# Kernel tuning notes

Measured on AMD Instinct MI355X. Metric: run time of the kernel, lower is better.

## Reference

```python
import jax, jax.numpy as jnp
import numpy as np

N_HEAD = 16


def setup_inputs() -> dict:
    key = jax.random.key(0)
    k1, k2, k3 = jax.random.split(key, 3)
    B, T, C = 4, 2048, 1024
    x = jax.random.normal(k1, (B, T, C), dtype=jnp.float32)
    W = jax.random.normal(k2, (3 * C, C), dtype=jnp.float32) * (1.0 / np.sqrt(C))
    b = jax.random.normal(k3, (3 * C,), dtype=jnp.float32) * 0.02
    return {"x": x, "W": W, "b": b, "input_pos": 0}


def reference(x, W, b, input_pos):
    # cache=False path; input_pos is unused (kept for signature fidelity).
    B, T, C = x.shape
    H = N_HEAD
    hs = C // H
    # Fused QKV projection: torch Linear is x @ W.T + b -> [B, T, 3C]
    qkv = (jnp.einsum('btc,oc->bto', x, W) + b).reshape(B, T, 3, H, hs)
    # q, k, v: [B, H, T, hs]
    q = jnp.transpose(qkv[:, :, 0], (0, 2, 1, 3))
    k = jnp.transpose(qkv[:, :, 1], (0, 2, 1, 3))
    v = jnp.transpose(qkv[:, :, 2], (0, 2, 1, 3))
    scale = hs ** (-0.5)
    # scores: [B, H, T, T]
    scores = jnp.einsum('bhqd,bhkd->bhqk', q, k) * scale
    causal = jnp.tril(jnp.ones((T, T), dtype=bool))
    scores = jnp.where(causal, scores, -jnp.inf)
    wei = jax.nn.softmax(scores, axis=-1)
    out = jnp.einsum('bhqk,bhkd->bhqd', wei, v)  # [B, H, T, hs]
    return jnp.transpose(out, (0, 2, 1, 3)).reshape(B, T, C)
```

## Files before the change

### kernel.cpp

```cpp
#include <hip/hip_runtime.h>
#include <stdint.h>

using s16x8 = __attribute__((ext_vector_type(8))) short;
using u16x8 = __attribute__((ext_vector_type(8))) unsigned short;
using f32x4 = __attribute__((ext_vector_type(4))) float;
using u32x2 = __attribute__((ext_vector_type(2))) uint32_t;

__device__ __forceinline__ unsigned short f2bf(float f) {
    union { float f; uint32_t u; } v; v.f = f;
    uint32_t u = (v.u + 0x7FFFu + ((v.u >> 16) & 1u)) >> 16;
    return (unsigned short)u;
}

#if defined(__has_builtin)
#if __has_builtin(__builtin_amdgcn_cvt_pk_bf16_f32)
#define HAS_PK_BF16 1
#endif
#if __has_builtin(__builtin_amdgcn_exp2f)
#define HAS_EXP2 1
#endif
#endif

__device__ __forceinline__ float ex2(float x) {
#ifdef HAS_EXP2
    return __builtin_amdgcn_exp2f(x);
#else
    float r; asm("v_exp_f32 %0, %1" : "=v"(r) : "v"(x)); return r;
#endif
}

__device__ __forceinline__ uint32_t pk2bf(float x, float y) {
#ifdef HAS_PK_BF16
    typedef __bf16 bf16x2 __attribute__((ext_vector_type(2)));
    union { bf16x2 v; uint32_t u; } c;
    c.v = __builtin_amdgcn_cvt_pk_bf16_f32(x, y);
    return c.u;
#else
    union { __bf16 v[2]; uint32_t u; } c;
    c.v[0] = (__bf16)x; c.v[1] = (__bf16)y;
    return c.u;
#endif
}

__device__ __forceinline__ f32x4 zero4() { f32x4 z = {0.f, 0.f, 0.f, 0.f}; return z; }

__device__ __forceinline__ void async16(const void* g, void* l) {
    __builtin_amdgcn_global_load_lds(
        reinterpret_cast<const uint32_t __attribute__((address_space(1)))*>(
            reinterpret_cast<uintptr_t>(g)),
        reinterpret_cast<uint32_t __attribute__((address_space(3)))*>(
            (uint32_t)reinterpret_cast<uintptr_t>(l)),
        16, 0, 0);
}

__global__ void cvt_bf16_2(const float* __restrict__ xa, unsigned short* __restrict__ oa, int na,
                           const float* __restrict__ xb, unsigned short* __restrict__ ob, int nb) {
    int i = (blockIdx.x * 256 + threadIdx.x) * 8;
    const float* in; unsigned short* out;
    if (i < na) { in = xa + i; out = oa + i; }
    else { int k = i - na; if (k >= nb) return; in = xb + k; out = ob + k; }
    f32x4 a = *(const f32x4*)(in);
    f32x4 c = *(const f32x4*)(in + 4);
    u16x8 o;
    o[0] = f2bf(a[0]); o[1] = f2bf(a[1]); o[2] = f2bf(a[2]); o[3] = f2bf(a[3]);
    o[4] = f2bf(c[0]); o[5] = f2bf(c[1]); o[6] = f2bf(c[2]); o[7] = f2bf(c[3]);
    *(u16x8*)(out) = o;
}

#define SC 0.18033688011112042f

__global__ __launch_bounds__(256, 2)
void qkv_gemm(const unsigned short* __restrict__ A,
              const unsigned short* __restrict__ Bw,
              const float* __restrict__ bias,
              unsigned short* __restrict__ Qo,
              unsigned short* __restrict__ Ko,
              unsigned short* __restrict__ Vto) {
    constexpr int Kd = 1024, T = 2048, H = 16;
    __shared__ __align__(16) unsigned short smem[128 * 136];
    unsigned short* const As = smem;
    unsigned short* const Bs = smem + 128 * 64;
    const int tid = threadIdx.x;
    const int wave = tid >> 6, lane = tid & 63;
    const int q4 = lane >> 4, l15 = lane & 15;
    const int bm = blockIdx.y * 128, bn = blockIdx.x * 128;
    const int wm = (wave >> 1) * 64, wn = (wave & 1) * 64;

    f32x4 acc[4][4];
#pragma unroll
    for (int a = 0; a < 4; ++a)
#pragma unroll
        for (int c = 0; c < 4; ++c) acc[a][c] = zero4();

    for (int k0 = 0; k0 < Kd; k0 += 64) {
#pragma unroll
        for (int r = 0; r < 4; ++r) {
            int u = r * 256 + tid;
            int row = u >> 3, su = (u & 7) ^ (row & 7);
            async16(A + (size_t)(bm + row) * Kd + k0 + su * 8, (char*)As + u * 16);
        }
#pragma unroll
        for (int r = 0; r < 4; ++r) {
            int u = r * 256 + tid;
            int row = u >> 3, su = (u & 7) ^ (row & 7);
            async16(Bw + (size_t)(bn + row) * Kd + k0 + su * 8, (char*)Bs + u * 16);
        }
        __syncthreads();
#pragma unroll
        for (int kt = 0; kt < 2; ++kt) {
            s16x8 af[4];
#pragma unroll
            for (int mt = 0; mt < 4; ++mt) {
                int row = wm + mt * 16 + l15;
                int uu = (kt * 4 + q4) ^ (row & 7);
                af[mt] = *(const s16x8*)(As + row * 64 + uu * 8);
            }
#pragma unroll
            for (int nt = 0; nt < 4; ++nt) {
                int row = wn + nt * 16 + l15;
                int uu = (kt * 4 + q4) ^ (row & 7);
                s16x8 bfv = *(const s16x8*)(Bs + row * 64 + uu * 8);
#pragma unroll
                for (int mt = 0; mt < 4; ++mt)
                    acc[mt][nt] = __builtin_amdgcn_mfma_f32_16x16x32_bf16(af[mt], bfv, acc[mt][nt], 0, 0, 0);
            }
        }
        __syncthreads();
    }
    if (bn >= 2048) {
#pragma unroll
        for (int nt = 0; nt < 4; ++nt) {
            int n = bn + wn + nt * 16 + l15;
            float bv = bias[n];
            int dl = wn + nt * 16 + l15;
#pragma unroll
            for (int mt = 0; mt < 4; ++mt)
#pragma unroll
                for (int i = 0; i < 4; ++i) {
                    int ml = wm + mt * 16 + 4 * q4 + i;
                    smem[dl * 136 + ml] = f2bf(acc[mt][nt][i] + bv);
                }
        }
        __syncthreads();
        const int bb = bm >> 11, t0 = bm & (T - 1);
#pragma unroll
        for (int rr = 0; rr < 8; ++rr) {
            int r = wave * 32 + rr * 4 + q4;
            int d = (bn - 2048) + r;
            int h = d >> 6, dd = d & 63;
            u16x8 v = *(const u16x8*)(smem + r * 136 + l15 * 8);
            *(u16x8*)(Vto + (((size_t)(bb * H + h)) * 64 + dd) * T + t0 + l15 * 8) = v;
        }
    } else {
#pragma unroll
        for (int nt = 0; nt < 4; ++nt) {
            int n = bn + wn + nt * 16 + l15;
            float bv = bias[n];
            int which = n >> 10, h = (n >> 6) & (H - 1), d = n & 63;
            unsigned short* dst = (which == 0) ? Qo : Ko;
            float scl = (which == 0) ? SC : 1.0f;
#pragma unroll
            for (int mt = 0; mt < 4; ++mt)
#pragma unroll
                for (int i = 0; i < 4; ++i) {
                    int m = bm + wm + mt * 16 + 4 * q4 + i;
                    int bb = m >> 11, t = m & (T - 1);
                    dst[((((size_t)bb * H + h) * T) + t) * 64 + d] = f2bf((acc[mt][nt][i] + bv) * scl);
                }
        }
    }
}

__global__ __launch_bounds__(256, 3)
void flash_attn(const unsigned short* __restrict__ Qg,
                const unsigned short* __restrict__ Kg,
                const unsigned short* __restrict__ Vtg,
                float* __restrict__ Out) {
    constexpr int T = 2048;
    __shared__ __align__(16) unsigned short Qs[128 * 64];
    __shared__ __align__(16) unsigned short Ks[2][64 * 64];
    __shared__ __align__(16) unsigned short Vt[2][64 * 64];

    const int tid = threadIdx.x;
    const int wave = tid >> 6, lane = tid & 63;
    const int q4 = lane >> 4, l15 = lane & 15;
    const int bh = blockIdx.x;
    const int qt = (int)gridDim.y - 1 - (int)blockIdx.y;
    const int b = bh >> 4, h = bh & 15;
    const int q0 = qt * 128;
    const unsigned short* qb = Qg + (size_t)bh * T * 64;
    const unsigned short* kb = Kg + (size_t)bh * T * 64;
    const unsigned short* vtb = Vtg + (size_t)bh * 64 * T;

#pragma unroll
    for (int r = 0; r < 4; ++r) {
        int u = r * 256 + tid;
        int row = u >> 3, su = (u & 7) ^ (row & 7);
        async16(qb + (size_t)(q0 + row) * 64 + su * 8, (char*)Qs + u * 16);
    }
#pragma unroll
    for (int r = 0; r < 2; ++r) {
        int u = r * 256 + tid;
        int row = u >> 3, su = (u & 7) ^ (row & 7);
        async16(kb + (size_t)row * 64 + su * 8, (char*)Ks[0] + u * 16);
        async16(vtb + (size_t)row * T + su * 8, (char*)Vt[0] + u * 16);
    }
    __syncthreads();
    s16x8 aq[2][2];
#pragma unroll
    for (int s = 0; s < 2; ++s)
#pragma unroll
        for (int kt = 0; kt < 2; ++kt) {
            int arow = s * 64 + wave * 16 + l15;
            int au = (kt * 4 + q4) ^ (arow & 7);
            aq[s][kt] = *(const s16x8*)(Qs + arow * 64 + au * 8);
        }
    __syncthreads();
    unsigned short* const Ps0 = Qs + (wave * 2 + 0) * 1024;
    unsigned short* const Ps1 = Qs + (wave * 2 + 1) * 1024;

    f32x4 oacc[2][4];
    float lsum[2] = {0.f, 0.f};
#pragma unroll
    for (int s = 0; s < 2; ++s)
#pragma unroll
        for (int ct = 0; ct < 4; ++ct) oacc[s][ct] = zero4();

    const int nkt = 2 * qt + 2;

    auto tile_step = [&](int j,
                         const unsigned short* __restrict__ kcur,
                         const unsigned short* __restrict__ vcur,
                         unsigned short* __restrict__ kd,
                         unsigned short* __restrict__ vd) {
        if (j + 1 < nkt) {
            const int cn = (j + 1) * 64;
#pragma unroll
            for (int r = 0; r < 2; ++r) {
                int u = r * 256 + tid;
                int row = u >> 3, su = (u & 7) ^ (row & 7);
                async16(kb + (size_t)(cn + row) * 64 + su * 8, (char*)kd + u * 16);
                async16(vtb + (size_t)row * T + cn + su * 8, (char*)vd + u * 16);
            }
        }
        const int c0 = j * 64;
        const bool alive0 = (j <= 2 * qt);

        f32x4 sv[2][4];
#pragma unroll
        for (int s = 0; s < 2; ++s)
#pragma unroll
            for (int t = 0; t < 4; ++t) sv[s][t] = zero4();
#pragma unroll
        for (int kt = 0; kt < 2; ++kt) {
#pragma unroll
            for (int t = 0; t < 4; ++t) {
                int krow = t * 16 + l15;
                int ku = (kt * 4 + q4) ^ (krow & 7);
                s16x8 ak = *(const s16x8*)(kcur + krow * 64 + ku * 8);
                sv[0][t] = __builtin_amdgcn_mfma_f32_16x16x32_bf16(ak, aq[0][kt], sv[0][t], 0, 0, 0);
                sv[1][t] = __builtin_amdgcn_mfma_f32_16x16x32_bf16(ak, aq[1][kt], sv[1][t], 0, 0, 0);
            }
        }

#pragma unroll
        for (int s = 0; s < 2; ++s) {
            if (s == 0 && !alive0) continue;
            const bool dg = (j == 2 * qt + s);
            unsigned short* const ps = (s == 0) ? Ps0 : Ps1;
            const int qrow = q0 + s * 64 + wave * 16 + l15;
#pragma unroll
            for (int t = 0; t < 4; ++t) {
                float p0 = ex2(sv[s][t][0]);
                float p1 = ex2(sv[s][t][1]);
                float p2 = ex2(sv[s][t][2]);
                float p3 = ex2(sv[s][t][3]);
                if (dg) {
                    int col = c0 + t * 16 + 4 * q4;
                    if (col + 0 > qrow) p0 = 0.f;
                    if (col + 1 > qrow) p1 = 0.f;
                    if (col + 2 > qrow) p2 = 0.f;
                    if (col + 3 > qrow) p3 = 0.f;
                }
                lsum[s] += (p0 + p1) + (p2 + p3);
                u32x2 w;
                w[0] = pk2bf(p0, p1);
                w[1] = pk2bf(p2, p3);
                *(u32x2*)(ps + l15 * 64 + (((2 * t + (q4 >> 1)) ^ (l15 & 7)) << 3) +
                          ((q4 & 1) << 2)) = w;
            }
        }

#pragma unroll
        for (int kt = 0; kt < 2; ++kt) {
            int pu = ((kt * 4 + q4) ^ (l15 & 7)) * 8;
            s16x8 pa0, pa1;
            if (alive0) pa0 = *(const s16x8*)(Ps0 + l15 * 64 + pu);
            pa1 = *(const s16x8*)(Ps1 + l15 * 64 + pu);
#pragma unroll
            for (int ct = 0; ct < 4; ++ct) {
                int vrow = ct * 16 + l15;
                int vu = (kt * 4 + q4) ^ (vrow & 7);
                s16x8 vv = *(const s16x8*)(vcur + vrow * 64 + vu * 8);
                if (alive0)
                    oacc[0][ct] = __builtin_amdgcn_mfma_f32_16x16x32_bf16(pa0, vv, oacc[0][ct], 0, 0, 0);
                oacc[1][ct] = __builtin_amdgcn_mfma_f32_16x16x32_bf16(pa1, vv, oacc[1][ct], 0, 0, 0);
            }
        }
        __syncthreads();
    };

    for (int j = 0; j < nkt; j += 2) {
        tile_step(j + 0, Ks[0], Vt[0], Ks[1], Vt[1]);
        tile_step(j + 1, Ks[1], Vt[1], Ks[0], Vt[0]);
    }

#pragma unroll
    for (int s = 0; s < 2; ++s) {
        float rs = lsum[s];
        rs += __shfl_xor(rs, 16, 64);
        rs += __shfl_xor(rs, 32, 64);
        float inv[4];
#pragma unroll
        for (int i = 0; i < 4; ++i)
            inv[i] = 1.0f / __shfl(rs, 4 * q4 + i, 64);
#pragma unroll
        for (int ct = 0; ct < 4; ++ct)
#pragma unroll
            for (int i = 0; i < 4; ++i) {
                int row = q0 + s * 64 + wave * 16 + 4 * q4 + i;
                Out[((size_t)b * T + row) * 1024 + h * 64 + ct * 16 + l15] =
                    oacc[s][ct][i] * inv[i];
            }
    }
}

extern "C" void kernel_launch(void* const* d_in, const int* in_sizes, int n_in,
                              void* d_out, int out_size, void* d_ws, size_t ws_size,
                              hipStream_t stream) {
    const float* x = (const float*)d_in[0];
    const float* W = (const float*)d_in[1];
    const float* bias = (const float*)d_in[2];
    float* out = (float*)d_out;

    unsigned short* xb = (unsigned short*)d_ws;
    unsigned short* wb = xb + 8388608;
    unsigned short* qb = wb + 3145728;
    unsigned short* kb = qb + 8388608;
    unsigned short* vtb = kb + 8388608;

    cvt_bf16_2<<<dim3((8388608 + 3145728) / 2048), dim3(256), 0, stream>>>(
        x, xb, 8388608, W, wb, 3145728);
    qkv_gemm<<<dim3(24, 64), dim3(256), 0, stream>>>(xb, wb, bias, qb, kb, vtb);
    flash_attn<<<dim3(64, 16), dim3(256), 0, stream>>>(qb, kb, vtb, out);
}
```

Baseline: 191.2 us.

## Switch flash attention to 32x32 MFMA with register-resident P and no Q LDS

```diff
diff --git a/kernel.cpp b/kernel.cpp
--- a/kernel.cpp
+++ b/kernel.cpp
@@ -2,8 +2,10 @@
 #include <stdint.h>
 
 using s16x8 = __attribute__((ext_vector_type(8))) short;
+using s16x4 = __attribute__((ext_vector_type(4))) short;
 using u16x8 = __attribute__((ext_vector_type(8))) unsigned short;
 using f32x4 = __attribute__((ext_vector_type(4))) float;
+using f32x16 = __attribute__((ext_vector_type(16))) float;
 using u32x2 = __attribute__((ext_vector_type(2))) uint32_t;
 
 __device__ __forceinline__ unsigned short f2bf(float f) {
@@ -171,33 +173,28 @@
     }
 }
 
-__global__ __launch_bounds__(256, 3)
+__global__ __launch_bounds__(256, 4)
 void flash_attn(const unsigned short* __restrict__ Qg,
                 const unsigned short* __restrict__ Kg,
                 const unsigned short* __restrict__ Vtg,
                 float* __restrict__ Out) {
     constexpr int T = 2048;
-    __shared__ __align__(16) unsigned short Qs[128 * 64];
     __shared__ __align__(16) unsigned short Ks[2][64 * 64];
     __shared__ __align__(16) unsigned short Vt[2][64 * 64];
 
     const int tid = threadIdx.x;
     const int wave = tid >> 6, lane = tid & 63;
-    const int q4 = lane >> 4, l15 = lane & 15;
+    const int l31 = lane & 31, hv = lane >> 5;
     const int bh = blockIdx.x;
     const int qt = (int)gridDim.y - 1 - (int)blockIdx.y;
-    const int b = bh >> 4, h = bh & 15;
+    const int b = bh >> 4, hh = bh & 15;
     const int q0 = qt * 128;
+    const int q_lo = q0 + wave * 32;
+    const int jlast = q_lo >> 6;
     const unsigned short* qb = Qg + (size_t)bh * T * 64;
     const unsigned short* kb = Kg + (size_t)bh * T * 64;
     const unsigned short* vtb = Vtg + (size_t)bh * 64 * T;
 
-#pragma unroll
-    for (int r = 0; r < 4; ++r) {
-        int u = r * 256 + tid;
-        int row = u >> 3, su = (u & 7) ^ (row & 7);
-        async16(qb + (size_t)(q0 + row) * 64 + su * 8, (char*)Qs + u * 16);
-    }
 #pragma unroll
     for (int r = 0; r < 2; ++r) {
         int u = r * 256 + tid;
@@ -205,26 +202,16 @@
         async16(kb + (size_t)row * 64 + su * 8, (char*)Ks[0] + u * 16);
         async16(vtb + (size_t)row * T + su * 8, (char*)Vt[0] + u * 16);
     }
+    s16x8 aq[4];
+#pragma unroll
+    for (int kt = 0; kt < 4; ++kt)
+        aq[kt] = *(const s16x8*)(qb + (size_t)(q_lo + l31) * 64 + kt * 16 + hv * 8);
     __syncthreads();
-    s16x8 aq[2][2];
-#pragma unroll
-    for (int s = 0; s < 2; ++s)
-#pragma unroll
-        for (int kt = 0; kt < 2; ++kt) {
-            int arow = s * 64 + wave * 16 + l15;
-            int au = (kt * 4 + q4) ^ (arow & 7);
-            aq[s][kt] = *(const s16x8*)(Qs + arow * 64 + au * 8);
-        }
-    __syncthreads();
-    unsigned short* const Ps0 = Qs + (wave * 2 + 0) * 1024;
-    unsigned short* const Ps1 = Qs + (wave * 2 + 1) * 1024;
-
-    f32x4 oacc[2][4];
-    float lsum[2] = {0.f, 0.f};
-#pragma unroll
-    for (int s = 0; s < 2; ++s)
-#pragma unroll
-        for (int ct = 0; ct < 4; ++ct) oacc[s][ct] = zero4();
+
+    f32x16 oacc[2];
+#pragma unroll
+    for (int i = 0; i < 16; ++i) { oacc[0][i] = 0.f; oacc[1][i] = 0.f; }
+    float lsum = 0.f;
 
     const int nkt = 2 * qt + 2;
 
@@ -243,68 +230,61 @@
                 async16(vtb + (size_t)row * T + cn + su * 8, (char*)vd + u * 16);
             }
         }
-        const int c0 = j * 64;
-        const bool alive0 = (j <= 2 * qt);
-
-        f32x4 sv[2][4];
-#pragma unroll
-        for (int s = 0; s < 2; ++s)
-#pragma unroll
-            for (int t = 0; t < 4; ++t) sv[s][t] = zero4();
-#pragma unroll
-        for (int kt = 0; kt < 2; ++kt) {
-#pragma unroll
-            for (int t = 0; t < 4; ++t) {
-                int krow = t * 16 + l15;
-                int ku = (kt * 4 + q4) ^ (krow & 7);
-                s16x8 ak = *(const s16x8*)(kcur + krow * 64 + ku * 8);
-                sv[0][t] = __builtin_amdgcn_mfma_f32_16x16x32_bf16(ak, aq[0][kt], sv[0][t], 0, 0, 0);
-                sv[1][t] = __builtin_amdgcn_mfma_f32_16x16x32_bf16(ak, aq[1][kt], sv[1][t], 0, 0, 0);
-            }
-        }
-
-#pragma unroll
-        for (int s = 0; s < 2; ++s) {
-            if (s == 0 && !alive0) continue;
-            const bool dg = (j == 2 * qt + s);
-            unsigned short* const ps = (s == 0) ? Ps0 : Ps1;
-            const int qrow = q0 + s * 64 + wave * 16 + l15;
-#pragma unroll
-            for (int t = 0; t < 4; ++t) {
-                float p0 = ex2(sv[s][t][0]);
-                float p1 = ex2(sv[s][t][1]);
-                float p2 = ex2(sv[s][t][2]);
-                float p3 = ex2(sv[s][t][3]);
-                if (dg) {
-                    int col = c0 + t * 16 + 4 * q4;
-                    if (col + 0 > qrow) p0 = 0.f;
-                    if (col + 1 > qrow) p1 = 0.f;
-                    if (col + 2 > qrow) p2 = 0.f;
-                    if (col + 3 > qrow) p3 = 0.f;
+        if (j <= jlast) {
+            f32x16 sv0, sv1;
+#pragma unroll
+            for (int i = 0; i < 16; ++i) { sv0[i] = 0.f; sv1[i] = 0.f; }
+#pragma unroll
+            for (int kt = 0; kt < 4; ++kt) {
+                int u = ((2 * kt + hv) ^ (l31 & 7)) * 8;
+                s16x8 ak0 = *(const s16x8*)(kcur + l31 * 64 + u);
+                s16x8 ak1 = *(const s16x8*)(kcur + (32 + l31) * 64 + u);
+                sv0 = __builtin_amdgcn_mfma_f32_32x32x16_bf16(ak0, aq[kt], sv0, 0, 0, 0);
+                sv1 = __builtin_amdgcn_mfma_f32_32x32x16_bf16(ak1, aq[kt], sv1, 0, 0, 0);
+            }
+
+#pragma unroll
+            for (int i = 0; i < 16; ++i) { sv0[i] = ex2(sv0[i]); sv1[i] = ex2(sv1[i]); }
+            if (j == jlast) {
+                const int marg = l31 + (q_lo - j * 64) - 4 * hv;
+#pragma unroll
+                for (int i = 0; i < 16; ++i) {
+                    int rr = (i & 3) + 8 * (i >> 2);
+                    if (rr > marg) sv0[i] = 0.f;
+                    if (rr + 32 > marg) sv1[i] = 0.f;
                 }
-                lsum[s] += (p0 + p1) + (p2 + p3);
-                u32x2 w;
-                w[0] = pk2bf(p0, p1);
-                w[1] = pk2bf(p2, p3);
-                *(u32x2*)(ps + l15 * 64 + (((2 * t + (q4 >> 1)) ^ (l15 & 7)) << 3) +
-                          ((q4 & 1) << 2)) = w;
-            }
-        }
-
-#pragma unroll
-        for (int kt = 0; kt < 2; ++kt) {
-            int pu = ((kt * 4 + q4) ^ (l15 & 7)) * 8;
-            s16x8 pa0, pa1;
-            if (alive0) pa0 = *(const s16x8*)(Ps0 + l15 * 64 + pu);
-            pa1 = *(const s16x8*)(Ps1 + l15 * 64 + pu);
-#pragma unroll
-            for (int ct = 0; ct < 4; ++ct) {
-                int vrow = ct * 16 + l15;
-                int vu = (kt * 4 + q4) ^ (vrow & 7);
-                s16x8 vv = *(const s16x8*)(vcur + vrow * 64 + vu * 8);
-                if (alive0)
-                    oacc[0][ct] = __builtin_amdgcn_mfma_f32_16x16x32_bf16(pa0, vv, oacc[0][ct], 0, 0, 0);
-                oacc[1][ct] = __builtin_amdgcn_mfma_f32_16x16x32_bf16(pa1, vv, oacc[1][ct], 0, 0, 0);
+            }
+            float ls0 = 0.f, ls1 = 0.f;
+#pragma unroll
+            for (int i = 0; i < 16; ++i) { ls0 += sv0[i]; ls1 += sv1[i]; }
+            lsum += ls0 + ls1;
+
+            uint32_t Dw0[4][2], Dw1[4][2];
+#pragma unroll
+            for (int a2 = 0; a2 < 4; ++a2) {
+                Dw0[a2][0] = pk2bf(sv0[4 * a2 + 0], sv0[4 * a2 + 1]);
+                Dw0[a2][1] = pk2bf(sv0[4 * a2 + 2], sv0[4 * a2 + 3]);
+                Dw1[a2][0] = pk2bf(sv1[4 * a2 + 0], sv1[4 * a2 + 1]);
+                Dw1[a2][1] = pk2bf(sv1[4 * a2 + 2], sv1[4 * a2 + 3]);
+            }
+
+#pragma unroll
+            for (int kt = 0; kt < 4; ++kt) {
+                const uint32_t* Dt = (kt < 2) ? &Dw0[0][0] : &Dw1[0][0];
+                union { uint32_t d[4]; s16x8 v; } pa;
+#pragma unroll
+                for (int c = 0; c < 4; ++c) pa.d[c] = Dt[4 * (kt & 1) + c];
+                const int o_lo = (((2 * kt + 0) ^ (l31 & 7)) * 16) + 8 * hv;
+                const int o_hi = (((2 * kt + 1) ^ (l31 & 7)) * 16) + 8 * hv;
+                const char* b0v = (const char*)vcur + l31 * 128;
+                const char* b1v = (const char*)vcur + (32 + l31) * 128;
+                union { s16x4 h[2]; s16x8 v; } vv0, vv1;
+                vv0.h[0] = *(const s16x4*)(b0v + o_lo);
+                vv0.h[1] = *(const s16x4*)(b0v + o_hi);
+                vv1.h[0] = *(const s16x4*)(b1v + o_lo);
+                vv1.h[1] = *(const s16x4*)(b1v + o_hi);
+                oacc[0] = __builtin_amdgcn_mfma_f32_32x32x16_bf16(pa.v, vv0.v, oacc[0], 0, 0, 0);
+                oacc[1] = __builtin_amdgcn_mfma_f32_32x32x16_bf16(pa.v, vv1.v, oacc[1], 0, 0, 0);
             }
         }
         __syncthreads();
@@ -315,23 +295,14 @@
         tile_step(j + 1, Ks[1], Vt[1], Ks[0], Vt[0]);
     }
 
-#pragma unroll
-    for (int s = 0; s < 2; ++s) {
-        float rs = lsum[s];
-        rs += __shfl_xor(rs, 16, 64);
-        rs += __shfl_xor(rs, 32, 64);
-        float inv[4];
-#pragma unroll
-        for (int i = 0; i < 4; ++i)
-            inv[i] = 1.0f / __shfl(rs, 4 * q4 + i, 64);
-#pragma unroll
-        for (int ct = 0; ct < 4; ++ct)
-#pragma unroll
-            for (int i = 0; i < 4; ++i) {
-                int row = q0 + s * 64 + wave * 16 + 4 * q4 + i;
-                Out[((size_t)b * T + row) * 1024 + h * 64 + ct * 16 + l15] =
-                    oacc[s][ct][i] * inv[i];
-            }
+    float rs = lsum + __shfl_xor(lsum, 32, 64);
+#pragma unroll
+    for (int i = 0; i < 16; ++i) {
+        int qlr = (i & 3) + 8 * (i >> 2) + 4 * hv;
+        float iv = 1.0f / __shfl(rs, qlr, 64);
+        float* op = Out + ((size_t)b * T + q_lo + qlr) * 1024 + hh * 64 + l31;
+        op[0]  = oacc[0][i] * iv;
+        op[32] = oacc[1][i] * iv;
     }
 }
 
```

New measurement: 199.5 us. +4.3%, slower.

## Rewrite QKV GEMM as 256x128 tile, 8-wave, double-buffered pipelined kernel

Applied to the files above, without the earlier changes.

```diff
diff --git a/kernel.cpp b/kernel.cpp
--- a/kernel.cpp
+++ b/kernel.cpp
@@ -52,6 +52,8 @@
             (uint32_t)reinterpret_cast<uintptr_t>(l)),
         16, 0, 0);
 }
+
+#define BARRIER() do { __builtin_amdgcn_s_barrier(); __builtin_amdgcn_sched_barrier(0); } while (0)
 
 __global__ void cvt_bf16_2(const float* __restrict__ xa, unsigned short* __restrict__ oa, int na,
                            const float* __restrict__ xb, unsigned short* __restrict__ ob, int nb) {
@@ -69,103 +71,164 @@
 
 #define SC 0.18033688011112042f
 
-__global__ __launch_bounds__(256, 2)
+__global__ __launch_bounds__(512, 2)
 void qkv_gemm(const unsigned short* __restrict__ A,
               const unsigned short* __restrict__ Bw,
               const float* __restrict__ bias,
               unsigned short* __restrict__ Qo,
               unsigned short* __restrict__ Ko,
               unsigned short* __restrict__ Vto) {
-    constexpr int Kd = 1024, T = 2048, H = 16;
-    __shared__ __align__(16) unsigned short smem[128 * 136];
-    unsigned short* const As = smem;
-    unsigned short* const Bs = smem + 128 * 64;
+    __shared__ __align__(16) unsigned short smem[49152];
     const int tid = threadIdx.x;
     const int wave = tid >> 6, lane = tid & 63;
     const int q4 = lane >> 4, l15 = lane & 15;
-    const int bm = blockIdx.y * 128, bn = blockIdx.x * 128;
-    const int wm = (wave >> 1) * 64, wn = (wave & 1) * 64;
-
-    f32x4 acc[4][4];
-#pragma unroll
-    for (int a = 0; a < 4; ++a)
-#pragma unroll
-        for (int c = 0; c < 4; ++c) acc[a][c] = zero4();
-
-    for (int k0 = 0; k0 < Kd; k0 += 64) {
-#pragma unroll
-        for (int r = 0; r < 4; ++r) {
-            int u = r * 256 + tid;
-            int row = u >> 3, su = (u & 7) ^ (row & 7);
-            async16(A + (size_t)(bm + row) * Kd + k0 + su * 8, (char*)As + u * 16);
-        }
-#pragma unroll
-        for (int r = 0; r < 4; ++r) {
-            int u = r * 256 + tid;
-            int row = u >> 3, su = (u & 7) ^ (row & 7);
-            async16(Bw + (size_t)(bn + row) * Kd + k0 + su * 8, (char*)Bs + u * 16);
+    const int bm = blockIdx.y * 256, bn = blockIdx.x * 128;
+    const int wrO = (wave >> 2) * 128;
+    const int wcO = (wave & 3) * 32;
+
+    auto stageA = [&](int t2, int h) {
+#pragma unroll
+        for (int r = 0; r < 2; ++r) {
+            int w = r * 512 + tid, row = w >> 3, su = (w & 7) ^ (row & 7);
+            async16(A + (size_t)(bm + h * 128 + row) * 1024 + t2 * 64 + su * 8,
+                    (char*)(smem + (t2 & 1) * 16384 + h * 8192) + w * 16);
+        }
+    };
+    auto stageB = [&](int t2, int g) {
+        int w = tid, row = w >> 3, su = (w & 7) ^ (row & 7);
+        async16(Bw + (size_t)(bn + g * 64 + row) * 1024 + t2 * 64 + su * 8,
+                (char*)(smem + 32768 + (t2 & 1) * 8192 + g * 4096) + w * 16);
+    };
+
+    f32x4 acc[8][2];
+#pragma unroll
+    for (int a = 0; a < 8; ++a) { acc[a][0] = zero4(); acc[a][1] = zero4(); }
+
+#pragma unroll
+    for (int t2 = 0; t2 < 2; ++t2) {
+        stageA(t2, 0); stageA(t2, 1);
+        stageB(t2, 0); stageB(t2, 1);
+    }
+    asm volatile("s_waitcnt vmcnt(0)" ::: "memory");
+    __syncthreads();
+
+#pragma unroll 2
+    for (int t = 0; t < 16; ++t) {
+        const unsigned short* As_s = smem + (t & 1) * 16384;
+        const unsigned short* Bs_s = smem + 32768 + (t & 1) * 8192;
+        s16x8 af[4][2], bf[2][2];
+#pragma unroll
+        for (int mf = 0; mf < 4; ++mf) {
+            const unsigned short* p = As_s + (wrO + mf * 16 + l15) * 64;
+#pragma unroll
+            for (int kt = 0; kt < 2; ++kt)
+                af[mf][kt] = *(const s16x8*)(p + (((kt * 4 + q4) ^ (l15 & 7)) << 3));
+        }
+        {
+            const unsigned short* p = Bs_s + (wcO + l15) * 64;
+#pragma unroll
+            for (int kt = 0; kt < 2; ++kt)
+                bf[0][kt] = *(const s16x8*)(p + (((kt * 4 + q4) ^ (l15 & 7)) << 3));
+        }
+        if (t >= 1 && t <= 14) stageA(t + 1, 1);
+        BARRIER();
+        __builtin_amdgcn_s_setprio(1);
+#pragma unroll
+        for (int kt = 0; kt < 2; ++kt)
+#pragma unroll
+            for (int mf = 0; mf < 4; ++mf)
+                acc[mf][0] = __builtin_amdgcn_mfma_f32_16x16x32_bf16(af[mf][kt], bf[0][kt], acc[mf][0], 0, 0, 0);
+        __builtin_amdgcn_s_setprio(0);
+        BARRIER();
+        {
+            const unsigned short* p = Bs_s + (wcO + 16 + l15) * 64;
+#pragma unroll
+            for (int kt = 0; kt < 2; ++kt)
+                bf[1][kt] = *(const s16x8*)(p + (((kt * 4 + q4) ^ (l15 & 7)) << 3));
+        }
+        BARRIER();
+        __builtin_amdgcn_s_setprio(1);
+#pragma unroll
+        for (int kt = 0; kt < 2; ++kt)
+#pragma unroll
+            for (int mf = 0; mf < 4; ++mf)
+                acc[mf][1] = __builtin_amdgcn_mfma_f32_16x16x32_bf16(af[mf][kt], bf[1][kt], acc[mf][1], 0, 0, 0);
+        __builtin_amdgcn_s_setprio(0);
+        BARRIER();
+#pragma unroll
+        for (int mf = 0; mf < 4; ++mf) {
+            const unsigned short* p = As_s + (wrO + 64 + mf * 16 + l15) * 64;
+#pragma unroll
+            for (int kt = 0; kt < 2; ++kt)
+                af[mf][kt] = *(const s16x8*)(p + (((kt * 4 + q4) ^ (l15 & 7)) << 3));
+        }
+        if (t <= 13) stageB(t + 2, 0);
+        BARRIER();
+        __builtin_amdgcn_s_setprio(1);
+#pragma unroll
+        for (int kt = 0; kt < 2; ++kt)
+#pragma unroll
+            for (int mf = 0; mf < 4; ++mf)
+                acc[4 + mf][1] = __builtin_amdgcn_mfma_f32_16x16x32_bf16(af[mf][kt], bf[1][kt], acc[4 + mf][1], 0, 0, 0);
+        __builtin_amdgcn_s_setprio(0);
+        BARRIER();
+        if (t <= 13) { stageB(t + 2, 1); stageA(t + 2, 0); }
+        BARRIER();
+        __builtin_amdgcn_s_setprio(1);
+#pragma unroll
+        for (int kt = 0; kt < 2; ++kt)
+#pragma unroll
+            for (int mf = 0; mf < 4; ++mf)
+                acc[4 + mf][0] = __builtin_amdgcn_mfma_f32_16x16x32_bf16(af[mf][kt], bf[0][kt], acc[4 + mf][0], 0, 0, 0);
+        __builtin_amdgcn_s_setprio(0);
+        if (t < 14) { asm volatile("s_waitcnt vmcnt(4)" ::: "memory"); }
+        else        { asm volatile("s_waitcnt vmcnt(0)" ::: "memory"); }
+        BARRIER();
+    }
+    __syncthreads();
+
+    if (bn >= 2048) {
+#pragma unroll
+        for (int nf = 0; nf < 2; ++nf) {
+            int n = bn + wcO + nf * 16 + l15;
+            float bv = bias[n];
+            int dl = wcO + nf * 16 + l15;
+#pragma unroll
+            for (int mf = 0; mf < 8; ++mf)
+#pragma unroll
+                for (int i = 0; i < 4; ++i) {
+                    int ml = wrO + mf * 16 + 4 * q4 + i;
+                    smem[dl * 264 + ml] = f2bf(acc[mf][nf][i] + bv);
+                }
         }
         __syncthreads();
-#pragma unroll
-        for (int kt = 0; kt < 2; ++kt) {
-            s16x8 af[4];
-#pragma unroll
-            for (int mt = 0; mt < 4; ++mt) {
-                int row = wm + mt * 16 + l15;
-                int uu = (kt * 4 + q4) ^ (row & 7);
-                af[mt] = *(const s16x8*)(As + row * 64 + uu * 8);
-            }
-#pragma unroll
-            for (int nt = 0; nt < 4; ++nt) {
-                int row = wn + nt * 16 + l15;
-                int uu = (kt * 4 + q4) ^ (row & 7);
-                s16x8 bfv = *(const s16x8*)(Bs + row * 64 + uu * 8);
-#pragma unroll
-                for (int mt = 0; mt < 4; ++mt)
-                    acc[mt][nt] = __builtin_amdgcn_mfma_f32_16x16x32_bf16(af[mt], bfv, acc[mt][nt], 0, 0, 0);
-            }
-        }
-        __syncthreads();
-    }
-    if (bn >= 2048) {
-#pragma unroll
-        for (int nt = 0; nt < 4; ++nt) {
-            int n = bn + wn + nt * 16 + l15;
-            float bv = bias[n];
-            int dl = wn + nt * 16 + l15;
-#pragma unroll
-            for (int mt = 0; mt < 4; ++mt)
-#pragma unroll
-                for (int i = 0; i < 4; ++i) {
-                    int ml = wm + mt * 16 + 4 * q4 + i;
-                    smem[dl * 136 + ml] = f2bf(acc[mt][nt][i] + bv);
-                }
-        }
-        __syncthreads();
-        const int bb = bm >> 11, t0 = bm & (T - 1);
-#pragma unroll
-        for (int rr = 0; rr < 8; ++rr) {
-            int r = wave * 32 + rr * 4 + q4;
+        const int bb = bm >> 11, t0 = bm & 2047;
+#pragma unroll
+        for (int rr = 0; rr < 4; ++rr) {
+            int r = wave * 16 + rr * 4 + q4;
             int d = (bn - 2048) + r;
             int h = d >> 6, dd = d & 63;
-            u16x8 v = *(const u16x8*)(smem + r * 136 + l15 * 8);
-            *(u16x8*)(Vto + (((size_t)(bb * H + h)) * 64 + dd) * T + t0 + l15 * 8) = v;
+#pragma unroll
+            for (int seg = 0; seg < 2; ++seg) {
+                u16x8 v = *(const u16x8*)(smem + r * 264 + seg * 128 + l15 * 8);
+                *(u16x8*)(Vto + (((size_t)(bb * 16 + h)) * 64 + dd) * 2048 + t0 + seg * 128 + l15 * 8) = v;
+            }
         }
     } else {
 #pragma unroll
-        for (int nt = 0; nt < 4; ++nt) {
-            int n = bn + wn + nt * 16 + l15;
+        for (int nf = 0; nf < 2; ++nf) {
+            int n = bn + wcO + nf * 16 + l15;
             float bv = bias[n];
-            int which = n >> 10, h = (n >> 6) & (H - 1), d = n & 63;
+            int which = n >> 10, h = (n >> 6) & 15, d = n & 63;
             unsigned short* dst = (which == 0) ? Qo : Ko;
             float scl = (which == 0) ? SC : 1.0f;
 #pragma unroll
-            for (int mt = 0; mt < 4; ++mt)
+            for (int mf = 0; mf < 8; ++mf)
 #pragma unroll
                 for (int i = 0; i < 4; ++i) {
-                    int m = bm + wm + mt * 16 + 4 * q4 + i;
-                    int bb = m >> 11, t = m & (T - 1);
-                    dst[((((size_t)bb * H + h) * T) + t) * 64 + d] = f2bf((acc[mt][nt][i] + bv) * scl);
+                    int m = bm + wrO + mf * 16 + 4 * q4 + i;
+                    int bb = m >> 11, tt = m & 2047;
+                    dst[((((size_t)bb * 16 + h) * 2048) + tt) * 64 + d] = f2bf((acc[mf][nf][i] + bv) * scl);
                 }
         }
     }
@@ -351,6 +414,6 @@
 
     cvt_bf16_2<<<dim3((8388608 + 3145728) / 2048), dim3(256), 0, stream>>>(
         x, xb, 8388608, W, wb, 3145728);
-    qkv_gemm<<<dim3(24, 64), dim3(256), 0, stream>>>(xb, wb, bias, qb, kb, vtb);
+    qkv_gemm<<<dim3(24, 32), dim3(512), 0, stream>>>(xb, wb, bias, qb, kb, vtb);
     flash_attn<<<dim3(64, 16), dim3(256), 0, stream>>>(qb, kb, vtb, out);
 }
```

After: 205.7 us. 1.08x slower.

## Keep P in registers and load Q directly, dropping the Q/P shared buffer

Applied to the files above, without the earlier changes.

```diff
diff --git a/kernel.cpp b/kernel.cpp
--- a/kernel.cpp
+++ b/kernel.cpp
@@ -2,6 +2,7 @@
 #include <stdint.h>
 
 using s16x8 = __attribute__((ext_vector_type(8))) short;
+using s16x4 = __attribute__((ext_vector_type(4))) short;
 using u16x8 = __attribute__((ext_vector_type(8))) unsigned short;
 using f32x4 = __attribute__((ext_vector_type(4))) float;
 using u32x2 = __attribute__((ext_vector_type(2))) uint32_t;
@@ -171,13 +172,12 @@
     }
 }
 
-__global__ __launch_bounds__(256, 3)
+__global__ __launch_bounds__(256, 4)
 void flash_attn(const unsigned short* __restrict__ Qg,
                 const unsigned short* __restrict__ Kg,
                 const unsigned short* __restrict__ Vtg,
                 float* __restrict__ Out) {
     constexpr int T = 2048;
-    __shared__ __align__(16) unsigned short Qs[128 * 64];
     __shared__ __align__(16) unsigned short Ks[2][64 * 64];
     __shared__ __align__(16) unsigned short Vt[2][64 * 64];
 
@@ -185,7 +185,8 @@
     const int wave = tid >> 6, lane = tid & 63;
     const int q4 = lane >> 4, l15 = lane & 15;
     const int bh = blockIdx.x;
-    const int qt = (int)gridDim.y - 1 - (int)blockIdx.y;
+    const int qtmap[16] = {15, 14, 13, 12, 8, 9, 10, 11, 7, 6, 5, 4, 0, 1, 2, 3};
+    const int qt = qtmap[blockIdx.y];
     const int b = bh >> 4, h = bh & 15;
     const int q0 = qt * 128;
     const unsigned short* qb = Qg + (size_t)bh * T * 64;
@@ -193,31 +194,20 @@
     const unsigned short* vtb = Vtg + (size_t)bh * 64 * T;
 
 #pragma unroll
-    for (int r = 0; r < 4; ++r) {
-        int u = r * 256 + tid;
-        int row = u >> 3, su = (u & 7) ^ (row & 7);
-        async16(qb + (size_t)(q0 + row) * 64 + su * 8, (char*)Qs + u * 16);
-    }
-#pragma unroll
     for (int r = 0; r < 2; ++r) {
         int u = r * 256 + tid;
         int row = u >> 3, su = (u & 7) ^ (row & 7);
         async16(kb + (size_t)row * 64 + su * 8, (char*)Ks[0] + u * 16);
         async16(vtb + (size_t)row * T + su * 8, (char*)Vt[0] + u * 16);
     }
+    s16x8 aq[2][2];
+#pragma unroll
+    for (int s = 0; s < 2; ++s)
+#pragma unroll
+        for (int kt = 0; kt < 2; ++kt)
+            aq[s][kt] = *(const s16x8*)(qb + (size_t)(q0 + s * 64 + wave * 16 + l15) * 64 +
+                                        kt * 32 + q4 * 8);
     __syncthreads();
-    s16x8 aq[2][2];
-#pragma unroll
-    for (int s = 0; s < 2; ++s)
-#pragma unroll
-        for (int kt = 0; kt < 2; ++kt) {
-            int arow = s * 64 + wave * 16 + l15;
-            int au = (kt * 4 + q4) ^ (arow & 7);
-            aq[s][kt] = *(const s16x8*)(Qs + arow * 64 + au * 8);
-        }
-    __syncthreads();
-    unsigned short* const Ps0 = Qs + (wave * 2 + 0) * 1024;
-    unsigned short* const Ps1 = Qs + (wave * 2 + 1) * 1024;
 
     f32x4 oacc[2][4];
     float lsum[2] = {0.f, 0.f};
@@ -267,7 +257,6 @@
         for (int s = 0; s < 2; ++s) {
             if (s == 0 && !alive0) continue;
             const bool dg = (j == 2 * qt + s);
-            unsigned short* const ps = (s == 0) ? Ps0 : Ps1;
             const int qrow = q0 + s * 64 + wave * 16 + l15;
 #pragma unroll
             for (int t = 0; t < 4; ++t) {
@@ -283,28 +272,37 @@
                     if (col + 3 > qrow) p3 = 0.f;
                 }
                 lsum[s] += (p0 + p1) + (p2 + p3);
-                u32x2 w;
-                w[0] = pk2bf(p0, p1);
-                w[1] = pk2bf(p2, p3);
-                *(u32x2*)(ps + l15 * 64 + (((2 * t + (q4 >> 1)) ^ (l15 & 7)) << 3) +
-                          ((q4 & 1) << 2)) = w;
+                sv[s][t][0] = p0; sv[s][t][1] = p1; sv[s][t][2] = p2; sv[s][t][3] = p3;
             }
         }
 
 #pragma unroll
         for (int kt = 0; kt < 2; ++kt) {
-            int pu = ((kt * 4 + q4) ^ (l15 & 7)) * 8;
-            s16x8 pa0, pa1;
-            if (alive0) pa0 = *(const s16x8*)(Ps0 + l15 * 64 + pu);
-            pa1 = *(const s16x8*)(Ps1 + l15 * 64 + pu);
+            union { uint32_t d[4]; s16x8 v; } pa0, pa1;
+            if (alive0) {
+                pa0.d[0] = pk2bf(sv[0][2 * kt][0], sv[0][2 * kt][1]);
+                pa0.d[1] = pk2bf(sv[0][2 * kt][2], sv[0][2 * kt][3]);
+                pa0.d[2] = pk2bf(sv[0][2 * kt + 1][0], sv[0][2 * kt + 1][1]);
+                pa0.d[3] = pk2bf(sv[0][2 * kt + 1][2], sv[0][2 * kt + 1][3]);
+            }
+            pa1.d[0] = pk2bf(sv[1][2 * kt][0], sv[1][2 * kt][1]);
+            pa1.d[1] = pk2bf(sv[1][2 * kt][2], sv[1][2 * kt][3]);
+            pa1.d[2] = pk2bf(sv[1][2 * kt + 1][0], sv[1][2 * kt + 1][1]);
+            pa1.d[3] = pk2bf(sv[1][2 * kt + 1][2], sv[1][2 * kt + 1][3]);
+            const int c_lo = 4 * kt + (q4 >> 1);
+            const int half = (q4 & 1) * 8;
 #pragma unroll
             for (int ct = 0; ct < 4; ++ct) {
-                int vrow = ct * 16 + l15;
-                int vu = (kt * 4 + q4) ^ (vrow & 7);
-                s16x8 vv = *(const s16x8*)(vcur + vrow * 64 + vu * 8);
+                const int d = ct * 16 + l15;
+                const char* vb = (const char*)vcur + d * 128;
+                const int jl = ((c_lo ^ (d & 7)) << 4) + half;
+                const int jh = (((c_lo + 2) ^ (d & 7)) << 4) + half;
+                union { s16x4 hh[2]; s16x8 v; } vv;
+                vv.hh[0] = *(const s16x4*)(vb + jl);
+                vv.hh[1] = *(const s16x4*)(vb + jh);
                 if (alive0)
-                    oacc[0][ct] = __builtin_amdgcn_mfma_f32_16x16x32_bf16(pa0, vv, oacc[0][ct], 0, 0, 0);
-                oacc[1][ct] = __builtin_amdgcn_mfma_f32_16x16x32_bf16(pa1, vv, oacc[1][ct], 0, 0, 0);
+                    oacc[0][ct] = __builtin_amdgcn_mfma_f32_16x16x32_bf16(pa0.v, vv.v, oacc[0][ct], 0, 0, 0);
+                oacc[1][ct] = __builtin_amdgcn_mfma_f32_16x16x32_bf16(pa1.v, vv.v, oacc[1][ct], 0, 0, 0);
             }
         }
         __syncthreads();
```

Result: slower. 208.4 us (+9.0%).
